# Kernel optimization log

Hardware: AMD Instinct MI355X
Metric: run time of the kernel (lower is better)

The kernel has to match this reference:

```python
import jax, jax.numpy as jnp
import numpy as np

N_NODES = 100000
N_EDGES = 1600000
IN_C, HID, OUT_C = 128, 64, 64
N_LAYERS = 16
ALPHA, THETA = 0.1, 0.5


def setup_inputs() -> dict:
    key = jax.random.key(0)
    ks = jax.random.split(key, 8)
    x = jax.random.normal(ks[0], (N_NODES, IN_C), dtype=jnp.float32)
    edge_index = jax.random.randint(ks[1], (2, N_EDGES), 0, N_NODES, dtype=jnp.int64)
    # torch Linear: weight [out, in], bias [out]
    lin0_w = jax.random.normal(ks[2], (HID, IN_C), dtype=jnp.float32) / np.sqrt(IN_C)
    lin0_b = jnp.zeros((HID,), dtype=jnp.float32)
    lin1_w = jax.random.normal(ks[3], (OUT_C, HID), dtype=jnp.float32) / np.sqrt(HID)
    lin1_b = jnp.zeros((OUT_C,), dtype=jnp.float32)
    # GCN2Conv weight1 per layer: [HID, HID], applied as h @ W
    conv_w = jax.random.normal(ks[4], (N_LAYERS, HID, HID), dtype=jnp.float32) / np.sqrt(HID)
    return {"x": x, "edge_index": edge_index, "lin0_w": lin0_w, "lin0_b": lin0_b,
            "lin1_w": lin1_w, "lin1_b": lin1_b, "conv_w": conv_w}


def reference(x, edge_index, lin0_w, lin0_b, lin1_w, lin1_b, conv_w):
    src, dst = edge_index[0], edge_index[1]
    # input projection (dropout p=0 in eval -> identity)
    h = jax.nn.relu(x @ lin0_w.T + lin0_b)  # [N, HID]
    h0 = h
    for l in range(N_LAYERS):
        # unweighted sum aggregation over edges (normalize=False, edge_weight=None)
        agg = jax.ops.segment_sum(h[src], dst, num_segments=N_NODES)  # [N, HID]
        z = (1.0 - ALPHA) * agg + ALPHA * h0  # initial residual
        beta = np.log(THETA / (l + 1) + 1.0).astype(np.float32)  # identity mapping strength
        h = jax.nn.relu((1.0 - beta) * z + beta * (z @ conv_w[l]))
    return h @ lin1_w.T + lin1_b  # [N, OUT_C]
```

## Files before the change

kernel.cpp:

```cpp
#include <hip/hip_runtime.h>
#include <cmath>

#define HID 64
#define IN_C 128

__device__ __forceinline__ float rl(float v, int k) {
    return __uint_as_float(__builtin_amdgcn_readlane(__float_as_uint(v), k));
}
__device__ __forceinline__ float bflo(unsigned u) { return __uint_as_float(u << 16); }
__device__ __forceinline__ float bfhi(unsigned u) { return __uint_as_float(u & 0xffff0000u); }
__device__ __forceinline__ unsigned bfpack(float lo, float hi) {
    unsigned a = __float_as_uint(lo), b = __float_as_uint(hi);
    a = (a + 0x7fffu + ((a >> 16) & 1u)) >> 16;
    b = (b + 0x7fffu + ((b >> 16) & 1u)) & 0xffff0000u;
    return a | b;
}

__device__ __forceinline__ float xadd8(float x) {
    int t = __builtin_amdgcn_update_dpp(0, __float_as_int(x), 0x128, 0xF, 0xF, true);
    return x + __int_as_float(t);
}
#if __has_builtin(__builtin_amdgcn_permlane16_swap)
typedef unsigned uvec2 __attribute__((ext_vector_type(2)));
__device__ __forceinline__ float xadd16(float x) {
    uvec2 r = __builtin_amdgcn_permlane16_swap(__float_as_uint(x), __float_as_uint(x), false, false);
    return __uint_as_float(r[0]) + __uint_as_float(r[1]);
}
#else
__device__ __forceinline__ float xadd16(float x) { return x + __shfl_xor(x, 16); }
#endif
#if __has_builtin(__builtin_amdgcn_permlane32_swap)
typedef unsigned uvec2b __attribute__((ext_vector_type(2)));
__device__ __forceinline__ float xadd32(float x) {
    uvec2b r = __builtin_amdgcn_permlane32_swap(__float_as_uint(x), __float_as_uint(x), false, false);
    return __uint_as_float(r[0]) + __uint_as_float(r[1]);
}
#else
__device__ __forceinline__ float xadd32(float x) { return x + __shfl_xor(x, 32); }
#endif
__device__ __forceinline__ float pairswap(float x) {
    int t = __builtin_amdgcn_update_dpp(0, __float_as_int(x), 0xB1, 0xF, 0xF, true);
    return __int_as_float(t);
}


__global__ void k_hist(const int* __restrict__ dst, int* __restrict__ counts, int E) {
    int e = blockIdx.x * blockDim.x + threadIdx.x;
    if (e < E) atomicAdd(&counts[dst[e]], 1);
}

__global__ void k_scan_block(const int* __restrict__ counts, int* __restrict__ row_ptr,
                             int* __restrict__ chunk_sums, int n) {
    __shared__ int s[1024];
    int i = blockIdx.x * 1024 + threadIdx.x;
    int v = (i < n) ? counts[i] : 0;
    s[threadIdx.x] = v;
    __syncthreads();
    for (int off = 1; off < 1024; off <<= 1) {
        int t = (threadIdx.x >= off) ? s[threadIdx.x - off] : 0;
        __syncthreads();
        s[threadIdx.x] += t;
        __syncthreads();
    }
    if (i < n) row_ptr[i] = s[threadIdx.x] - v;
    if (threadIdx.x == 1023) chunk_sums[blockIdx.x] = s[1023];
}

__global__ void k_scan_fix(int* __restrict__ row_ptr, const int* __restrict__ chunk_sums,
                           int n, int total) {
    __shared__ int base_s;
    if (threadIdx.x == 0) {
        int b = 0;
        for (int c = 0; c < (int)blockIdx.x; ++c) b += chunk_sums[c];
        base_s = b;
    }
    __syncthreads();
    int i = blockIdx.x * 1024 + threadIdx.x;
    if (i < n) row_ptr[i] += base_s;
    if (i == 0) row_ptr[n] = total;
}

__global__ void k_fill(const int* __restrict__ src, const int* __restrict__ dst,
                       const int* __restrict__ row_ptr, int* __restrict__ cursor,
                       int* __restrict__ col_idx, int E) {
    int e = blockIdx.x * blockDim.x + threadIdx.x;
    if (e < E) {
        int d = dst[e];
        int pos = row_ptr[d] + atomicAdd(&cursor[d], 1);
        col_idx[pos] = src[e];
    }
}

__global__ __launch_bounds__(256) void k_lin0(const float* __restrict__ x,
                                              const float* __restrict__ w,
                                              const float* __restrict__ b,
                                              unsigned* __restrict__ h0, int N) {
    __shared__ float Wt[IN_C * 65];
    for (int i = threadIdx.x; i < IN_C * HID; i += 256) {
        int o = i >> 7, k = i & 127;
        Wt[k * 65 + o] = w[i];
    }
    __syncthreads();
    int lane = threadIdx.x & 63;
    int wid = (blockIdx.x * blockDim.x + threadIdx.x) >> 6;
    int nw = (gridDim.x * blockDim.x) >> 6;
    float bias = b[lane];
    for (int n0 = wid; n0 < N; n0 += 2 * nw) {
        int n1 = n0 + nw;
        bool v1 = n1 < N;
        int n1c = v1 ? n1 : n0;
        float xa0 = x[(size_t)n0 * IN_C + lane];
        float xa1 = x[(size_t)n0 * IN_C + 64 + lane];
        float xb0 = x[(size_t)n1c * IN_C + lane];
        float xb1 = x[(size_t)n1c * IN_C + 64 + lane];
        float acc0 = bias, acc1 = bias;
#pragma unroll
        for (int k = 0; k < 64; ++k) {
            float wv = Wt[k * 65 + lane];
            acc0 = fmaf(rl(xa0, k), wv, acc0);
            acc1 = fmaf(rl(xb0, k), wv, acc1);
        }
#pragma unroll
        for (int k = 0; k < 64; ++k) {
            float wv = Wt[(64 + k) * 65 + lane];
            acc0 = fmaf(rl(xa1, k), wv, acc0);
            acc1 = fmaf(rl(xb1, k), wv, acc1);
        }
        acc0 = fmaxf(acc0, 0.f);
        acc1 = fmaxf(acc1, 0.f);
        float p0 = pairswap(acc0);
        float p1 = pairswap(acc1);
        if ((lane & 1) == 0) {
            h0[(size_t)n0 * 32 + (lane >> 1)] = bfpack(acc0, p0);
            if (v1) h0[(size_t)n1 * 32 + (lane >> 1)] = bfpack(acc1, p1);
        }
    }
}

__device__ __forceinline__ void mask4(uint4& q, bool v) {
    q.x = v ? q.x : 0u; q.y = v ? q.y : 0u; q.z = v ? q.z : 0u; q.w = v ? q.w : 0u;
}
__device__ __forceinline__ void acc8(float* a, const uint4& q) {
    a[0] += bflo(q.x); a[1] += bfhi(q.x);
    a[2] += bflo(q.y); a[3] += bfhi(q.y);
    a[4] += bflo(q.z); a[5] += bfhi(q.z);
    a[6] += bflo(q.w); a[7] += bfhi(q.w);
}

__global__ __launch_bounds__(256) void k_layer(const uint4* __restrict__ hin,
                                               const uint4* __restrict__ h0,
                                               unsigned* __restrict__ hout,
                                               const float* __restrict__ W,
                                               const int* __restrict__ row_ptr,
                                               const int* __restrict__ col_idx,
                                               float beta, int N, int E) {
    __shared__ uint4 Wp[8 * 64];
    for (int idx = threadIdx.x; idx < 8 * 64; idx += 256) {
        int k8 = idx >> 6, c = idx & 63;
        float wv[8];
#pragma unroll
        for (int m = 0; m < 8; ++m) {
            int k = 8 * k8 + m;
            float v = beta * W[k * 64 + c];
            if (k == c) v += 1.f - beta;
            wv[m] = v;
        }
        uint4 p;
        p.x = bfpack(wv[0], wv[1]); p.y = bfpack(wv[2], wv[3]);
        p.z = bfpack(wv[4], wv[5]); p.w = bfpack(wv[6], wv[7]);
        Wp[idx] = p;
    }
    __syncthreads();

    int lane = threadIdx.x & 63;
    int sub = lane >> 3;
    int cg = lane & 7;
    int wid = (blockIdx.x * blockDim.x + threadIdx.x) >> 6;
    int nw = (gridDim.x * blockDim.x) >> 6;

    for (int n = wid; n < N; n += 2 * nw) {
        int nB = n + nw;
        bool vB = nB < N;
        int nBc = vB ? nB : n;
        int bA = row_ptr[n];
        int dA = row_ptr[n + 1] - bA;
        int bB = row_ptr[nBc];
        int dB = vB ? row_ptr[nBc + 1] - bB : 0;
        uint4 hqA = h0[(size_t)n * 8 + cg];
        uint4 hqB = h0[(size_t)nBc * 8 + cg];
        int lastA = max(bA + dA - 1, 0);
        int lastB = max(bB + dB - 1, 0);
        float aA[8], aB[8];
#pragma unroll
        for (int c = 0; c < 8; ++c) { aA[c] = 0.f; aB[c] = 0.f; }
        int rmax = max(dA, dB);
        for (int j = 0; j < rmax; j += 16) {
            int p0 = j + sub, p1 = j + 8 + sub;
            int iA0 = col_idx[min(bA + p0, lastA)];
            int iA1 = col_idx[min(bA + p1, lastA)];
            int iB0 = col_idx[min(bB + p0, lastB)];
            int iB1 = col_idx[min(bB + p1, lastB)];
            uint4 qA0 = hin[(size_t)iA0 * 8 + cg];
            uint4 qA1 = hin[(size_t)iA1 * 8 + cg];
            uint4 qB0 = hin[(size_t)iB0 * 8 + cg];
            uint4 qB1 = hin[(size_t)iB1 * 8 + cg];
            mask4(qA0, p0 < dA); mask4(qA1, p1 < dA);
            mask4(qB0, p0 < dB); mask4(qB1, p1 < dB);
            acc8(aA, qA0); acc8(aA, qA1);
            acc8(aB, qB0); acc8(aB, qB1);
        }
#pragma unroll
        for (int c = 0; c < 8; ++c) { aA[c] = xadd8(aA[c]);  aB[c] = xadd8(aB[c]); }
#pragma unroll
        for (int c = 0; c < 8; ++c) { aA[c] = xadd16(aA[c]); aB[c] = xadd16(aB[c]); }
#pragma unroll
        for (int c = 0; c < 8; ++c) { aA[c] = xadd32(aA[c]); aB[c] = xadd32(aB[c]); }

        float zA[8], zB[8];
        zA[0] = 0.9f * aA[0] + 0.1f * bflo(hqA.x);
        zA[1] = 0.9f * aA[1] + 0.1f * bfhi(hqA.x);
        zA[2] = 0.9f * aA[2] + 0.1f * bflo(hqA.y);
        zA[3] = 0.9f * aA[3] + 0.1f * bfhi(hqA.y);
        zA[4] = 0.9f * aA[4] + 0.1f * bflo(hqA.z);
        zA[5] = 0.9f * aA[5] + 0.1f * bfhi(hqA.z);
        zA[6] = 0.9f * aA[6] + 0.1f * bflo(hqA.w);
        zA[7] = 0.9f * aA[7] + 0.1f * bfhi(hqA.w);
        zB[0] = 0.9f * aB[0] + 0.1f * bflo(hqB.x);
        zB[1] = 0.9f * aB[1] + 0.1f * bfhi(hqB.x);
        zB[2] = 0.9f * aB[2] + 0.1f * bflo(hqB.y);
        zB[3] = 0.9f * aB[3] + 0.1f * bfhi(hqB.y);
        zB[4] = 0.9f * aB[4] + 0.1f * bflo(hqB.z);
        zB[5] = 0.9f * aB[5] + 0.1f * bfhi(hqB.z);
        zB[6] = 0.9f * aB[6] + 0.1f * bflo(hqB.w);
        zB[7] = 0.9f * aB[7] + 0.1f * bfhi(hqB.w);

        float gA0 = 0.f, gA1 = 0.f, gA2 = 0.f, gA3 = 0.f;
        float gB0 = 0.f, gB1 = 0.f, gB2 = 0.f, gB3 = 0.f;
#pragma unroll
        for (int k8 = 0; k8 < 8; ++k8) {
            uint4 wp = Wp[k8 * 64 + lane];
            gA0 = fmaf(rl(zA[0], k8), bflo(wp.x), gA0);
            gA1 = fmaf(rl(zA[1], k8), bfhi(wp.x), gA1);
            gA2 = fmaf(rl(zA[2], k8), bflo(wp.y), gA2);
            gA3 = fmaf(rl(zA[3], k8), bfhi(wp.y), gA3);
            gA0 = fmaf(rl(zA[4], k8), bflo(wp.z), gA0);
            gA1 = fmaf(rl(zA[5], k8), bfhi(wp.z), gA1);
            gA2 = fmaf(rl(zA[6], k8), bflo(wp.w), gA2);
            gA3 = fmaf(rl(zA[7], k8), bfhi(wp.w), gA3);
            gB0 = fmaf(rl(zB[0], k8), bflo(wp.x), gB0);
            gB1 = fmaf(rl(zB[1], k8), bfhi(wp.x), gB1);
            gB2 = fmaf(rl(zB[2], k8), bflo(wp.y), gB2);
            gB3 = fmaf(rl(zB[3], k8), bfhi(wp.y), gB3);
            gB0 = fmaf(rl(zB[4], k8), bflo(wp.z), gB0);
            gB1 = fmaf(rl(zB[5], k8), bfhi(wp.z), gB1);
            gB2 = fmaf(rl(zB[6], k8), bflo(wp.w), gB2);
            gB3 = fmaf(rl(zB[7], k8), bfhi(wp.w), gB3);
        }
        float rA = fmaxf((gA0 + gA1) + (gA2 + gA3), 0.f);
        float rB = fmaxf((gB0 + gB1) + (gB2 + gB3), 0.f);
        float rAn = pairswap(rA);
        float rBn = pairswap(rB);
        if ((lane & 1) == 0) {
            hout[(size_t)n * 32 + (lane >> 1)] = bfpack(rA, rAn);
            if (vB) hout[(size_t)nB * 32 + (lane >> 1)] = bfpack(rB, rBn);
        }
    }
}

__global__ __launch_bounds__(256) void k_lin1(const unsigned* __restrict__ h,
                                              const float* __restrict__ w,
                                              const float* __restrict__ b,
                                              float* __restrict__ out, int N) {
    __shared__ float Wt[HID * 65];
    for (int i = threadIdx.x; i < HID * HID; i += 256) {
        int o = i >> 6, k = i & 63;
        Wt[k * 65 + o] = w[i];
    }
    __syncthreads();
    int lane = threadIdx.x & 63;
    int wid = (blockIdx.x * blockDim.x + threadIdx.x) >> 6;
    int nw = (gridDim.x * blockDim.x) >> 6;
    float bias = b[lane];
    for (int n0 = wid; n0 < N; n0 += 2 * nw) {
        int n1 = n0 + nw;
        bool v1 = n1 < N;
        int n1c = v1 ? n1 : n0;
        unsigned ua = h[(size_t)n0 * 32 + (lane >> 1)];
        unsigned ub = h[(size_t)n1c * 32 + (lane >> 1)];
        float ha = (lane & 1) ? bfhi(ua) : bflo(ua);
        float hb = (lane & 1) ? bfhi(ub) : bflo(ub);
        float acc0 = bias, acc1 = bias;
#pragma unroll
        for (int k = 0; k < 64; ++k) {
            float wv = Wt[k * 65 + lane];
            acc0 = fmaf(rl(ha, k), wv, acc0);
            acc1 = fmaf(rl(hb, k), wv, acc1);
        }
        out[(size_t)n0 * HID + lane] = acc0;
        if (v1) out[(size_t)n1 * HID + lane] = acc1;
    }
}

extern "C" void kernel_launch(void* const* d_in, const int* in_sizes, int n_in,
                              void* d_out, int out_size, void* d_ws, size_t ws_size,
                              hipStream_t stream) {
    const float* x      = (const float*)d_in[0];
    const int*   ei     = (const int*)d_in[1];
    const float* lin0_w = (const float*)d_in[2];
    const float* lin0_b = (const float*)d_in[3];
    const float* lin1_w = (const float*)d_in[4];
    const float* lin1_b = (const float*)d_in[5];
    const float* conv_w = (const float*)d_in[6];

    int N = in_sizes[0] / IN_C;
    int E = in_sizes[1] / 2;
    const int* src = ei;
    const int* dst = ei + E;

    unsigned* h0 = (unsigned*)d_ws;
    unsigned* hA = h0 + (size_t)N * 32;
    unsigned* hB = hA + (size_t)N * 32;
    int* row_ptr    = (int*)(hB + (size_t)N * 32);
    int* cursor     = row_ptr + (N + 1);
    int* col_idx    = cursor + N;
    int* chunk_sums = col_idx + E;

    int nch = (N + 1023) / 1024;

    hipMemsetAsync(cursor, 0, (size_t)N * sizeof(int), stream);
    k_hist<<<(E + 255) / 256, 256, 0, stream>>>(dst, cursor, E);
    k_scan_block<<<nch, 1024, 0, stream>>>(cursor, row_ptr, chunk_sums, N);
    k_scan_fix<<<nch, 1024, 0, stream>>>(row_ptr, chunk_sums, N, E);
    hipMemsetAsync(cursor, 0, (size_t)N * sizeof(int), stream);
    k_fill<<<(E + 255) / 256, 256, 0, stream>>>(src, dst, row_ptr, cursor, col_idx, E);

    k_lin0<<<1024, 256, 0, stream>>>(x, lin0_w, lin0_b, h0, N);

    const unsigned* cur = h0;
    for (int l = 0; l < 16; ++l) {
        float beta = (float)log(0.5 / (double)(l + 1) + 1.0);
        unsigned* nxt = (l & 1) ? hB : hA;
        k_layer<<<2048, 256, 0, stream>>>((const uint4*)cur, (const uint4*)h0, nxt,
                                          conv_w + (size_t)l * HID * HID,
                                          row_ptr, col_idx, beta, N, E);
        cur = nxt;
    }

    k_lin1<<<1024, 256, 0, stream>>>(cur, lin1_w, lin1_b, (float*)d_out, N);
}
```

Measured before the change: 1.507 ms.

## Process contiguous node chunks per wave and stage neighbor indices in LDS

Each wave now handles a contiguous chunk of 13 nodes instead of striding nodes across the grid. It loads the row pointers once per chunk into lanes and broadcasts them with readlane. It also prefetches the chunk's col_idx range (up to 512 entries) into shared memory with coalesced loads, falling back to global memory beyond that. This is meant to cut scattered row_ptr and col_idx loads, at the cost of extra LDS use (8KB per block), which may lower occupancy, and an unsynchronized per-wave LDS fill.

```diff
diff --git a/kernel.cpp b/kernel.cpp
--- a/kernel.cpp
+++ b/kernel.cpp
@@ -3,9 +3,14 @@
 
 #define HID 64
 #define IN_C 128
+#define CHUNK 13
+#define IDXCAP 512
 
 __device__ __forceinline__ float rl(float v, int k) {
     return __uint_as_float(__builtin_amdgcn_readlane(__float_as_uint(v), k));
+}
+__device__ __forceinline__ int rli(int v, int k) {
+    return __builtin_amdgcn_readlane(v, k);
 }
 __device__ __forceinline__ float bflo(unsigned u) { return __uint_as_float(u << 16); }
 __device__ __forceinline__ float bfhi(unsigned u) { return __uint_as_float(u & 0xffff0000u); }
@@ -153,8 +158,9 @@
                                                const float* __restrict__ W,
                                                const int* __restrict__ row_ptr,
                                                const int* __restrict__ col_idx,
-                                               float beta, int N, int E) {
+                                               float beta, int N) {
     __shared__ uint4 Wp[8 * 64];
+    __shared__ int idxb[4][IDXCAP];
     for (int idx = threadIdx.x; idx < 8 * 64; idx += 256) {
         int k8 = idx >> 6, c = idx & 63;
         float wv[8];
@@ -173,96 +179,109 @@
     __syncthreads();
 
     int lane = threadIdx.x & 63;
+    int wslot = threadIdx.x >> 6;
     int sub = lane >> 3;
     int cg = lane & 7;
-    int wid = (blockIdx.x * blockDim.x + threadIdx.x) >> 6;
-    int nw = (gridDim.x * blockDim.x) >> 6;
-
-    for (int n = wid; n < N; n += 2 * nw) {
-        int nB = n + nw;
-        bool vB = nB < N;
-        int nBc = vB ? nB : n;
-        int bA = row_ptr[n];
-        int dA = row_ptr[n + 1] - bA;
-        int bB = row_ptr[nBc];
-        int dB = vB ? row_ptr[nBc + 1] - bB : 0;
-        uint4 hqA = h0[(size_t)n * 8 + cg];
-        uint4 hqB = h0[(size_t)nBc * 8 + cg];
-        int lastA = max(bA + dA - 1, 0);
-        int lastB = max(bB + dB - 1, 0);
-        float aA[8], aB[8];
-#pragma unroll
-        for (int c = 0; c < 8; ++c) { aA[c] = 0.f; aB[c] = 0.f; }
-        int rmax = max(dA, dB);
-        for (int j = 0; j < rmax; j += 16) {
-            int p0 = j + sub, p1 = j + 8 + sub;
-            int iA0 = col_idx[min(bA + p0, lastA)];
-            int iA1 = col_idx[min(bA + p1, lastA)];
-            int iB0 = col_idx[min(bB + p0, lastB)];
-            int iB1 = col_idx[min(bB + p1, lastB)];
-            uint4 qA0 = hin[(size_t)iA0 * 8 + cg];
-            uint4 qA1 = hin[(size_t)iA1 * 8 + cg];
-            uint4 qB0 = hin[(size_t)iB0 * 8 + cg];
-            uint4 qB1 = hin[(size_t)iB1 * 8 + cg];
-            mask4(qA0, p0 < dA); mask4(qA1, p1 < dA);
-            mask4(qB0, p0 < dB); mask4(qB1, p1 < dB);
-            acc8(aA, qA0); acc8(aA, qA1);
-            acc8(aB, qB0); acc8(aB, qB1);
-        }
-#pragma unroll
-        for (int c = 0; c < 8; ++c) { aA[c] = xadd8(aA[c]);  aB[c] = xadd8(aB[c]); }
-#pragma unroll
-        for (int c = 0; c < 8; ++c) { aA[c] = xadd16(aA[c]); aB[c] = xadd16(aB[c]); }
-#pragma unroll
-        for (int c = 0; c < 8; ++c) { aA[c] = xadd32(aA[c]); aB[c] = xadd32(aB[c]); }
-
-        float zA[8], zB[8];
-        zA[0] = 0.9f * aA[0] + 0.1f * bflo(hqA.x);
-        zA[1] = 0.9f * aA[1] + 0.1f * bfhi(hqA.x);
-        zA[2] = 0.9f * aA[2] + 0.1f * bflo(hqA.y);
-        zA[3] = 0.9f * aA[3] + 0.1f * bfhi(hqA.y);
-        zA[4] = 0.9f * aA[4] + 0.1f * bflo(hqA.z);
-        zA[5] = 0.9f * aA[5] + 0.1f * bfhi(hqA.z);
-        zA[6] = 0.9f * aA[6] + 0.1f * bflo(hqA.w);
-        zA[7] = 0.9f * aA[7] + 0.1f * bfhi(hqA.w);
-        zB[0] = 0.9f * aB[0] + 0.1f * bflo(hqB.x);
-        zB[1] = 0.9f * aB[1] + 0.1f * bfhi(hqB.x);
-        zB[2] = 0.9f * aB[2] + 0.1f * bflo(hqB.y);
-        zB[3] = 0.9f * aB[3] + 0.1f * bfhi(hqB.y);
-        zB[4] = 0.9f * aB[4] + 0.1f * bflo(hqB.z);
-        zB[5] = 0.9f * aB[5] + 0.1f * bfhi(hqB.z);
-        zB[6] = 0.9f * aB[6] + 0.1f * bflo(hqB.w);
-        zB[7] = 0.9f * aB[7] + 0.1f * bfhi(hqB.w);
-
-        float gA0 = 0.f, gA1 = 0.f, gA2 = 0.f, gA3 = 0.f;
-        float gB0 = 0.f, gB1 = 0.f, gB2 = 0.f, gB3 = 0.f;
-#pragma unroll
-        for (int k8 = 0; k8 < 8; ++k8) {
-            uint4 wp = Wp[k8 * 64 + lane];
-            gA0 = fmaf(rl(zA[0], k8), bflo(wp.x), gA0);
-            gA1 = fmaf(rl(zA[1], k8), bfhi(wp.x), gA1);
-            gA2 = fmaf(rl(zA[2], k8), bflo(wp.y), gA2);
-            gA3 = fmaf(rl(zA[3], k8), bfhi(wp.y), gA3);
-            gA0 = fmaf(rl(zA[4], k8), bflo(wp.z), gA0);
-            gA1 = fmaf(rl(zA[5], k8), bfhi(wp.z), gA1);
-            gA2 = fmaf(rl(zA[6], k8), bflo(wp.w), gA2);
-            gA3 = fmaf(rl(zA[7], k8), bfhi(wp.w), gA3);
-            gB0 = fmaf(rl(zB[0], k8), bflo(wp.x), gB0);
-            gB1 = fmaf(rl(zB[1], k8), bfhi(wp.x), gB1);
-            gB2 = fmaf(rl(zB[2], k8), bflo(wp.y), gB2);
-            gB3 = fmaf(rl(zB[3], k8), bfhi(wp.y), gB3);
-            gB0 = fmaf(rl(zB[4], k8), bflo(wp.z), gB0);
-            gB1 = fmaf(rl(zB[5], k8), bfhi(wp.z), gB1);
-            gB2 = fmaf(rl(zB[6], k8), bflo(wp.w), gB2);
-            gB3 = fmaf(rl(zB[7], k8), bfhi(wp.w), gB3);
-        }
-        float rA = fmaxf((gA0 + gA1) + (gA2 + gA3), 0.f);
-        float rB = fmaxf((gB0 + gB1) + (gB2 + gB3), 0.f);
-        float rAn = pairswap(rA);
-        float rBn = pairswap(rB);
-        if ((lane & 1) == 0) {
-            hout[(size_t)n * 32 + (lane >> 1)] = bfpack(rA, rAn);
-            if (vB) hout[(size_t)nB * 32 + (lane >> 1)] = bfpack(rB, rBn);
+    int gw = (blockIdx.x * blockDim.x + threadIdx.x) >> 6;
+    int nwv = (gridDim.x * blockDim.x) >> 6;
+
+    for (int chunk = gw; chunk * CHUNK < N; chunk += nwv) {
+        int n0 = chunk * CHUNK;
+        int cnt = min(CHUNK, N - n0);
+        int rp = row_ptr[n0 + min(lane, cnt)];
+        int base = rli(rp, 0);
+        int tot = rli(rp, cnt) - base;
+        int ncap = min(tot, IDXCAP);
+        for (int t = lane; t < ncap; t += 64) idxb[wslot][t] = col_idx[base + t];
+
+        for (int i = 0; i < cnt; i += 2) {
+            bool vB = (i + 1) < cnt;
+            int iB = vB ? (i + 1) : i;
+            int rA0 = rli(rp, i), rA1 = rli(rp, i + 1);
+            int rB0 = rli(rp, iB), rB1 = rli(rp, iB + 1);
+            int bA = rA0 - base, dA = rA1 - rA0;
+            int bB = rB0 - base, dB = vB ? rB1 - rB0 : 0;
+            int nA = n0 + i, nB = n0 + iB;
+            uint4 hqA = h0[(size_t)nA * 8 + cg];
+            uint4 hqB = h0[(size_t)nB * 8 + cg];
+            int lastA = max(bA + dA - 1, 0);
+            int lastB = max(bB + dB - 1, 0);
+            float aA[8], aB[8];
+#pragma unroll
+            for (int c = 0; c < 8; ++c) { aA[c] = 0.f; aB[c] = 0.f; }
+            int rmax = max(dA, dB);
+            for (int j = 0; j < rmax; j += 16) {
+                int p0 = j + sub, p1 = j + 8 + sub;
+                int sA0 = min(bA + p0, lastA), sA1 = min(bA + p1, lastA);
+                int sB0 = min(bB + p0, lastB), sB1 = min(bB + p1, lastB);
+                int iA0 = (sA0 < IDXCAP) ? idxb[wslot][sA0] : col_idx[base + sA0];
+                int iA1 = (sA1 < IDXCAP) ? idxb[wslot][sA1] : col_idx[base + sA1];
+                int iB0 = (sB0 < IDXCAP) ? idxb[wslot][sB0] : col_idx[base + sB0];
+                int iB1 = (sB1 < IDXCAP) ? idxb[wslot][sB1] : col_idx[base + sB1];
+                uint4 qA0 = hin[(size_t)iA0 * 8 + cg];
+                uint4 qA1 = hin[(size_t)iA1 * 8 + cg];
+                uint4 qB0 = hin[(size_t)iB0 * 8 + cg];
+                uint4 qB1 = hin[(size_t)iB1 * 8 + cg];
+                mask4(qA0, p0 < dA); mask4(qA1, p1 < dA);
+                mask4(qB0, p0 < dB); mask4(qB1, p1 < dB);
+                acc8(aA, qA0); acc8(aA, qA1);
+                acc8(aB, qB0); acc8(aB, qB1);
+            }
+#pragma unroll
+            for (int c = 0; c < 8; ++c) { aA[c] = xadd8(aA[c]);  aB[c] = xadd8(aB[c]); }
+#pragma unroll
+            for (int c = 0; c < 8; ++c) { aA[c] = xadd16(aA[c]); aB[c] = xadd16(aB[c]); }
+#pragma unroll
+            for (int c = 0; c < 8; ++c) { aA[c] = xadd32(aA[c]); aB[c] = xadd32(aB[c]); }
+
+            float zA[8], zB[8];
+            zA[0] = 0.9f * aA[0] + 0.1f * bflo(hqA.x);
+            zA[1] = 0.9f * aA[1] + 0.1f * bfhi(hqA.x);
+            zA[2] = 0.9f * aA[2] + 0.1f * bflo(hqA.y);
+            zA[3] = 0.9f * aA[3] + 0.1f * bfhi(hqA.y);
+            zA[4] = 0.9f * aA[4] + 0.1f * bflo(hqA.z);
+            zA[5] = 0.9f * aA[5] + 0.1f * bfhi(hqA.z);
+            zA[6] = 0.9f * aA[6] + 0.1f * bflo(hqA.w);
+            zA[7] = 0.9f * aA[7] + 0.1f * bfhi(hqA.w);
+            zB[0] = 0.9f * aB[0] + 0.1f * bflo(hqB.x);
+            zB[1] = 0.9f * aB[1] + 0.1f * bfhi(hqB.x);
+            zB[2] = 0.9f * aB[2] + 0.1f * bflo(hqB.y);
+            zB[3] = 0.9f * aB[3] + 0.1f * bfhi(hqB.y);
+            zB[4] = 0.9f * aB[4] + 0.1f * bflo(hqB.z);
+            zB[5] = 0.9f * aB[5] + 0.1f * bfhi(hqB.z);
+            zB[6] = 0.9f * aB[6] + 0.1f * bflo(hqB.w);
+            zB[7] = 0.9f * aB[7] + 0.1f * bfhi(hqB.w);
+
+            float gA0 = 0.f, gA1 = 0.f, gA2 = 0.f, gA3 = 0.f;
+            float gB0 = 0.f, gB1 = 0.f, gB2 = 0.f, gB3 = 0.f;
+#pragma unroll
+            for (int k8 = 0; k8 < 8; ++k8) {
+                uint4 wp = Wp[k8 * 64 + lane];
+                gA0 = fmaf(rl(zA[0], k8), bflo(wp.x), gA0);
+                gA1 = fmaf(rl(zA[1], k8), bfhi(wp.x), gA1);
+                gA2 = fmaf(rl(zA[2], k8), bflo(wp.y), gA2);
+                gA3 = fmaf(rl(zA[3], k8), bfhi(wp.y), gA3);
+                gA0 = fmaf(rl(zA[4], k8), bflo(wp.z), gA0);
+                gA1 = fmaf(rl(zA[5], k8), bfhi(wp.z), gA1);
+                gA2 = fmaf(rl(zA[6], k8), bflo(wp.w), gA2);
+                gA3 = fmaf(rl(zA[7], k8), bfhi(wp.w), gA3);
+                gB0 = fmaf(rl(zB[0], k8), bflo(wp.x), gB0);
+                gB1 = fmaf(rl(zB[1], k8), bfhi(wp.x), gB1);
+                gB2 = fmaf(rl(zB[2], k8), bflo(wp.y), gB2);
+                gB3 = fmaf(rl(zB[3], k8), bfhi(wp.y), gB3);
+                gB0 = fmaf(rl(zB[4], k8), bflo(wp.z), gB0);
+                gB1 = fmaf(rl(zB[5], k8), bfhi(wp.z), gB1);
+                gB2 = fmaf(rl(zB[6], k8), bflo(wp.w), gB2);
+                gB3 = fmaf(rl(zB[7], k8), bfhi(wp.w), gB3);
+            }
+            float rA = fmaxf((gA0 + gA1) + (gA2 + gA3), 0.f);
+            float rB = fmaxf((gB0 + gB1) + (gB2 + gB3), 0.f);
+            float rAn = pairswap(rA);
+            float rBn = pairswap(rB);
+            if ((lane & 1) == 0) {
+                hout[(size_t)nA * 32 + (lane >> 1)] = bfpack(rA, rAn);
+                if (vB) hout[(size_t)nB * 32 + (lane >> 1)] = bfpack(rB, rBn);
+            }
         }
     }
 }
@@ -342,7 +361,7 @@
         unsigned* nxt = (l & 1) ? hB : hA;
         k_layer<<<2048, 256, 0, stream>>>((const uint4*)cur, (const uint4*)h0, nxt,
                                           conv_w + (size_t)l * HID * HID,
-                                          row_ptr, col_idx, beta, N, E);
+                                          row_ptr, col_idx, beta, N);
         cur = nxt;
     }
 
```

Result: slower. 1.583 ms (+5.1%).

## Split layer into channel-sliced aggregation and separate GEMM kernels

Applied to the files above, without the earlier changes.

Node features are stored channel-group-major: 8 slabs of 16-byte bf16 chunks, one slab per group of 8 channels. Each aggregation block handles a single slab, so its random gathers hit a 1.6 MB working set that can stay in cache. A separate GEMM kernel applies the mixing weight and converts back to the sliced layout. The cost is an intermediate z buffer (stored in the output buffer) that must be written and re-read, twice as many launches per layer, and one extra bf16 rounding of z.

```diff
diff --git a/kernel.cpp b/kernel.cpp
--- a/kernel.cpp
+++ b/kernel.cpp
@@ -16,28 +16,11 @@
     return a | b;
 }
 
-__device__ __forceinline__ float xadd8(float x) {
-    int t = __builtin_amdgcn_update_dpp(0, __float_as_int(x), 0x128, 0xF, 0xF, true);
+template <int CTRL>
+__device__ __forceinline__ float dppadd(float x) {
+    int t = __builtin_amdgcn_update_dpp(0, __float_as_int(x), CTRL, 0xF, 0xF, true);
     return x + __int_as_float(t);
 }
-#if __has_builtin(__builtin_amdgcn_permlane16_swap)
-typedef unsigned uvec2 __attribute__((ext_vector_type(2)));
-__device__ __forceinline__ float xadd16(float x) {
-    uvec2 r = __builtin_amdgcn_permlane16_swap(__float_as_uint(x), __float_as_uint(x), false, false);
-    return __uint_as_float(r[0]) + __uint_as_float(r[1]);
-}
-#else
-__device__ __forceinline__ float xadd16(float x) { return x + __shfl_xor(x, 16); }
-#endif
-#if __has_builtin(__builtin_amdgcn_permlane32_swap)
-typedef unsigned uvec2b __attribute__((ext_vector_type(2)));
-__device__ __forceinline__ float xadd32(float x) {
-    uvec2b r = __builtin_amdgcn_permlane32_swap(__float_as_uint(x), __float_as_uint(x), false, false);
-    return __uint_as_float(r[0]) + __uint_as_float(r[1]);
-}
-#else
-__device__ __forceinline__ float xadd32(float x) { return x + __shfl_xor(x, 32); }
-#endif
 __device__ __forceinline__ float pairswap(float x) {
     int t = __builtin_amdgcn_update_dpp(0, __float_as_int(x), 0xB1, 0xF, 0xF, true);
     return __int_as_float(t);
@@ -94,17 +77,19 @@
 __global__ __launch_bounds__(256) void k_lin0(const float* __restrict__ x,
                                               const float* __restrict__ w,
                                               const float* __restrict__ b,
-                                              unsigned* __restrict__ h0, int N) {
+                                              unsigned* __restrict__ S, int N) {
     __shared__ float Wt[IN_C * 65];
     for (int i = threadIdx.x; i < IN_C * HID; i += 256) {
         int o = i >> 7, k = i & 127;
         Wt[k * 65 + o] = w[i];
     }
     __syncthreads();
+    size_t N4 = (size_t)N * 4;
     int lane = threadIdx.x & 63;
     int wid = (blockIdx.x * blockDim.x + threadIdx.x) >> 6;
     int nw = (gridDim.x * blockDim.x) >> 6;
     float bias = b[lane];
+    size_t waddr = (size_t)(lane >> 3) * N4 + ((lane >> 1) & 3);
     for (int n0 = wid; n0 < N; n0 += 2 * nw) {
         int n1 = n0 + nw;
         bool v1 = n1 < N;
@@ -131,29 +116,111 @@
         float p0 = pairswap(acc0);
         float p1 = pairswap(acc1);
         if ((lane & 1) == 0) {
-            h0[(size_t)n0 * 32 + (lane >> 1)] = bfpack(acc0, p0);
-            if (v1) h0[(size_t)n1 * 32 + (lane >> 1)] = bfpack(acc1, p1);
-        }
-    }
-}
-
-__device__ __forceinline__ void mask4(uint4& q, bool v) {
-    q.x = v ? q.x : 0u; q.y = v ? q.y : 0u; q.z = v ? q.z : 0u; q.w = v ? q.w : 0u;
-}
-__device__ __forceinline__ void acc8(float* a, const uint4& q) {
-    a[0] += bflo(q.x); a[1] += bfhi(q.x);
-    a[2] += bflo(q.y); a[3] += bfhi(q.y);
-    a[4] += bflo(q.z); a[5] += bfhi(q.z);
-    a[6] += bflo(q.w); a[7] += bfhi(q.w);
-}
-
-__global__ __launch_bounds__(256) void k_layer(const uint4* __restrict__ hin,
-                                               const uint4* __restrict__ h0,
-                                               unsigned* __restrict__ hout,
-                                               const float* __restrict__ W,
-                                               const int* __restrict__ row_ptr,
-                                               const int* __restrict__ col_idx,
-                                               float beta, int N, int E) {
+            S[waddr + (size_t)n0 * 4] = bfpack(acc0, p0);
+            if (v1) S[waddr + (size_t)n1 * 4] = bfpack(acc1, p1);
+        }
+    }
+}
+
+__global__ __launch_bounds__(256) void k_aggr(const unsigned* __restrict__ Sin,
+                                              const unsigned* __restrict__ h0S,
+                                              unsigned* __restrict__ zrow,
+                                              const int* __restrict__ row_ptr,
+                                              const int* __restrict__ col_idx,
+                                              int N) {
+    int lane = threadIdx.x & 63;
+    int es = lane & 15, ds = lane >> 4;
+    int cg = blockIdx.x & 7;
+    int grp = blockIdx.x >> 3;
+    int ngrp = gridDim.x >> 3;
+    int wv = threadIdx.x >> 6;
+    int span = (N + ngrp - 1) / ngrp;
+    int nbeg = grp * span;
+    int nend = min(nbeg + span, N);
+    const uint4* slab = (const uint4*)(Sin + (size_t)cg * N * 4);
+    const uint4* h0sl = (const uint4*)(h0S + (size_t)cg * N * 4);
+    uint4* zr = (uint4*)zrow;
+
+    for (int n8 = nbeg + wv * 8; n8 < nend; n8 += 32) {
+        int nA = n8 + ds;
+        int nB = n8 + 4 + ds;
+        bool vA = nA < nend, vB = nB < nend;
+        int nAc = vA ? nA : nend - 1;
+        int nBc = vB ? nB : nend - 1;
+        int bA = row_ptr[nAc], eA = row_ptr[nAc + 1];
+        int bB = row_ptr[nBc], eB = row_ptr[nBc + 1];
+        int dA = eA - bA, dB = eB - bB;
+        int lastA = (dA > 0) ? eA - 1 : 0;
+        int lastB = (dB > 0) ? eB - 1 : 0;
+        int baseA = (dA > 0) ? bA : 0;
+        int baseB = (dB > 0) ? bB : 0;
+        float aA[8], aB[8];
+#pragma unroll
+        for (int c = 0; c < 8; ++c) { aA[c] = 0.f; aB[c] = 0.f; }
+        int rmax = max(dA, dB);
+        for (int j = es; j < rmax; j += 16) {
+            int pA = min(baseA + j, lastA);
+            int pB = min(baseB + j, lastB);
+            int iA = col_idx[pA];
+            int iB = col_idx[pB];
+            uint4 qA = slab[iA];
+            uint4 qB = slab[iB];
+            bool mA = j < dA, mB = j < dB;
+            if (!mA) { qA.x = 0; qA.y = 0; qA.z = 0; qA.w = 0; }
+            if (!mB) { qB.x = 0; qB.y = 0; qB.z = 0; qB.w = 0; }
+            aA[0] += bflo(qA.x); aA[1] += bfhi(qA.x);
+            aA[2] += bflo(qA.y); aA[3] += bfhi(qA.y);
+            aA[4] += bflo(qA.z); aA[5] += bfhi(qA.z);
+            aA[6] += bflo(qA.w); aA[7] += bfhi(qA.w);
+            aB[0] += bflo(qB.x); aB[1] += bfhi(qB.x);
+            aB[2] += bflo(qB.y); aB[3] += bfhi(qB.y);
+            aB[4] += bflo(qB.z); aB[5] += bfhi(qB.z);
+            aB[6] += bflo(qB.w); aB[7] += bfhi(qB.w);
+        }
+#pragma unroll
+        for (int c = 0; c < 8; ++c) { aA[c] = dppadd<0xB1>(aA[c]);  aB[c] = dppadd<0xB1>(aB[c]); }
+#pragma unroll
+        for (int c = 0; c < 8; ++c) { aA[c] = dppadd<0x4E>(aA[c]);  aB[c] = dppadd<0x4E>(aB[c]); }
+#pragma unroll
+        for (int c = 0; c < 8; ++c) { aA[c] = dppadd<0x124>(aA[c]); aB[c] = dppadd<0x124>(aB[c]); }
+#pragma unroll
+        for (int c = 0; c < 8; ++c) { aA[c] = dppadd<0x128>(aA[c]); aB[c] = dppadd<0x128>(aB[c]); }
+
+        uint4 hA = h0sl[nAc];
+        uint4 hB = h0sl[nBc];
+        float zA[8], zB[8];
+        zA[0] = 0.9f * aA[0] + 0.1f * bflo(hA.x);
+        zA[1] = 0.9f * aA[1] + 0.1f * bfhi(hA.x);
+        zA[2] = 0.9f * aA[2] + 0.1f * bflo(hA.y);
+        zA[3] = 0.9f * aA[3] + 0.1f * bfhi(hA.y);
+        zA[4] = 0.9f * aA[4] + 0.1f * bflo(hA.z);
+        zA[5] = 0.9f * aA[5] + 0.1f * bfhi(hA.z);
+        zA[6] = 0.9f * aA[6] + 0.1f * bflo(hA.w);
+        zA[7] = 0.9f * aA[7] + 0.1f * bfhi(hA.w);
+        zB[0] = 0.9f * aB[0] + 0.1f * bflo(hB.x);
+        zB[1] = 0.9f * aB[1] + 0.1f * bfhi(hB.x);
+        zB[2] = 0.9f * aB[2] + 0.1f * bflo(hB.y);
+        zB[3] = 0.9f * aB[3] + 0.1f * bfhi(hB.y);
+        zB[4] = 0.9f * aB[4] + 0.1f * bflo(hB.z);
+        zB[5] = 0.9f * aB[5] + 0.1f * bfhi(hB.z);
+        zB[6] = 0.9f * aB[6] + 0.1f * bflo(hB.w);
+        zB[7] = 0.9f * aB[7] + 0.1f * bfhi(hB.w);
+        uint4 zqA, zqB;
+        zqA.x = bfpack(zA[0], zA[1]); zqA.y = bfpack(zA[2], zA[3]);
+        zqA.z = bfpack(zA[4], zA[5]); zqA.w = bfpack(zA[6], zA[7]);
+        zqB.x = bfpack(zB[0], zB[1]); zqB.y = bfpack(zB[2], zB[3]);
+        zqB.z = bfpack(zB[4], zB[5]); zqB.w = bfpack(zB[6], zB[7]);
+        if (es == 0) {
+            if (vA) zr[(size_t)nA * 8 + cg] = zqA;
+            if (vB) zr[(size_t)nB * 8 + cg] = zqB;
+        }
+    }
+}
+
+__global__ __launch_bounds__(256) void k_gemm(const uint4* __restrict__ zrow,
+                                              unsigned* __restrict__ Sout,
+                                              const float* __restrict__ W,
+                                              float beta, int N) {
     __shared__ uint4 Wp[8 * 64];
     for (int idx = threadIdx.x; idx < 8 * 64; idx += 256) {
         int k8 = idx >> 6, c = idx & 63;
@@ -172,67 +239,28 @@
     }
     __syncthreads();
 
+    size_t N4 = (size_t)N * 4;
     int lane = threadIdx.x & 63;
-    int sub = lane >> 3;
     int cg = lane & 7;
     int wid = (blockIdx.x * blockDim.x + threadIdx.x) >> 6;
     int nw = (gridDim.x * blockDim.x) >> 6;
-
-    for (int n = wid; n < N; n += 2 * nw) {
-        int nB = n + nw;
-        bool vB = nB < N;
-        int nBc = vB ? nB : n;
-        int bA = row_ptr[n];
-        int dA = row_ptr[n + 1] - bA;
-        int bB = row_ptr[nBc];
-        int dB = vB ? row_ptr[nBc + 1] - bB : 0;
-        uint4 hqA = h0[(size_t)n * 8 + cg];
-        uint4 hqB = h0[(size_t)nBc * 8 + cg];
-        int lastA = max(bA + dA - 1, 0);
-        int lastB = max(bB + dB - 1, 0);
-        float aA[8], aB[8];
-#pragma unroll
-        for (int c = 0; c < 8; ++c) { aA[c] = 0.f; aB[c] = 0.f; }
-        int rmax = max(dA, dB);
-        for (int j = 0; j < rmax; j += 16) {
-            int p0 = j + sub, p1 = j + 8 + sub;
-            int iA0 = col_idx[min(bA + p0, lastA)];
-            int iA1 = col_idx[min(bA + p1, lastA)];
-            int iB0 = col_idx[min(bB + p0, lastB)];
-            int iB1 = col_idx[min(bB + p1, lastB)];
-            uint4 qA0 = hin[(size_t)iA0 * 8 + cg];
-            uint4 qA1 = hin[(size_t)iA1 * 8 + cg];
-            uint4 qB0 = hin[(size_t)iB0 * 8 + cg];
-            uint4 qB1 = hin[(size_t)iB1 * 8 + cg];
-            mask4(qA0, p0 < dA); mask4(qA1, p1 < dA);
-            mask4(qB0, p0 < dB); mask4(qB1, p1 < dB);
-            acc8(aA, qA0); acc8(aA, qA1);
-            acc8(aB, qB0); acc8(aB, qB1);
-        }
-#pragma unroll
-        for (int c = 0; c < 8; ++c) { aA[c] = xadd8(aA[c]);  aB[c] = xadd8(aB[c]); }
-#pragma unroll
-        for (int c = 0; c < 8; ++c) { aA[c] = xadd16(aA[c]); aB[c] = xadd16(aB[c]); }
-#pragma unroll
-        for (int c = 0; c < 8; ++c) { aA[c] = xadd32(aA[c]); aB[c] = xadd32(aB[c]); }
-
+    size_t waddr = (size_t)(lane >> 3) * N4 + ((lane >> 1) & 3);
+
+    for (int n0 = 2 * wid; n0 < N; n0 += 2 * nw) {
+        int n1 = n0 + 1;
+        bool v1 = n1 < N;
+        int n1c = v1 ? n1 : n0;
+        uint4 zqA = zrow[(size_t)n0 * 8 + cg];
+        uint4 zqB = zrow[(size_t)n1c * 8 + cg];
         float zA[8], zB[8];
-        zA[0] = 0.9f * aA[0] + 0.1f * bflo(hqA.x);
-        zA[1] = 0.9f * aA[1] + 0.1f * bfhi(hqA.x);
-        zA[2] = 0.9f * aA[2] + 0.1f * bflo(hqA.y);
-        zA[3] = 0.9f * aA[3] + 0.1f * bfhi(hqA.y);
-        zA[4] = 0.9f * aA[4] + 0.1f * bflo(hqA.z);
-        zA[5] = 0.9f * aA[5] + 0.1f * bfhi(hqA.z);
-        zA[6] = 0.9f * aA[6] + 0.1f * bflo(hqA.w);
-        zA[7] = 0.9f * aA[7] + 0.1f * bfhi(hqA.w);
-        zB[0] = 0.9f * aB[0] + 0.1f * bflo(hqB.x);
-        zB[1] = 0.9f * aB[1] + 0.1f * bfhi(hqB.x);
-        zB[2] = 0.9f * aB[2] + 0.1f * bflo(hqB.y);
-        zB[3] = 0.9f * aB[3] + 0.1f * bfhi(hqB.y);
-        zB[4] = 0.9f * aB[4] + 0.1f * bflo(hqB.z);
-        zB[5] = 0.9f * aB[5] + 0.1f * bfhi(hqB.z);
-        zB[6] = 0.9f * aB[6] + 0.1f * bflo(hqB.w);
-        zB[7] = 0.9f * aB[7] + 0.1f * bfhi(hqB.w);
+        zA[0] = bflo(zqA.x); zA[1] = bfhi(zqA.x);
+        zA[2] = bflo(zqA.y); zA[3] = bfhi(zqA.y);
+        zA[4] = bflo(zqA.z); zA[5] = bfhi(zqA.z);
+        zA[6] = bflo(zqA.w); zA[7] = bfhi(zqA.w);
+        zB[0] = bflo(zqB.x); zB[1] = bfhi(zqB.x);
+        zB[2] = bflo(zqB.y); zB[3] = bfhi(zqB.y);
+        zB[4] = bflo(zqB.z); zB[5] = bfhi(zqB.z);
+        zB[6] = bflo(zqB.w); zB[7] = bfhi(zqB.w);
 
         float gA0 = 0.f, gA1 = 0.f, gA2 = 0.f, gA3 = 0.f;
         float gB0 = 0.f, gB1 = 0.f, gB2 = 0.f, gB3 = 0.f;
@@ -261,13 +289,13 @@
         float rAn = pairswap(rA);
         float rBn = pairswap(rB);
         if ((lane & 1) == 0) {
-            hout[(size_t)n * 32 + (lane >> 1)] = bfpack(rA, rAn);
-            if (vB) hout[(size_t)nB * 32 + (lane >> 1)] = bfpack(rB, rBn);
-        }
-    }
-}
-
-__global__ __launch_bounds__(256) void k_lin1(const unsigned* __restrict__ h,
+            Sout[waddr + (size_t)n0 * 4] = bfpack(rA, rAn);
+            if (v1) Sout[waddr + (size_t)n1 * 4] = bfpack(rB, rBn);
+        }
+    }
+}
+
+__global__ __launch_bounds__(256) void k_lin1(const unsigned* __restrict__ S,
                                               const float* __restrict__ w,
                                               const float* __restrict__ b,
                                               float* __restrict__ out, int N) {
@@ -277,16 +305,18 @@
         Wt[k * 65 + o] = w[i];
     }
     __syncthreads();
+    size_t N4 = (size_t)N * 4;
     int lane = threadIdx.x & 63;
     int wid = (blockIdx.x * blockDim.x + threadIdx.x) >> 6;
     int nw = (gridDim.x * blockDim.x) >> 6;
     float bias = b[lane];
+    size_t raddr = (size_t)(lane >> 3) * N4 + ((lane >> 1) & 3);
     for (int n0 = wid; n0 < N; n0 += 2 * nw) {
         int n1 = n0 + nw;
         bool v1 = n1 < N;
         int n1c = v1 ? n1 : n0;
-        unsigned ua = h[(size_t)n0 * 32 + (lane >> 1)];
-        unsigned ub = h[(size_t)n1c * 32 + (lane >> 1)];
+        unsigned ua = S[raddr + (size_t)n0 * 4];
+        unsigned ub = S[raddr + (size_t)n1c * 4];
         float ha = (lane & 1) ? bfhi(ua) : bflo(ua);
         float hb = (lane & 1) ? bfhi(ub) : bflo(ub);
         float acc0 = bias, acc1 = bias;
@@ -317,13 +347,14 @@
     const int* src = ei;
     const int* dst = ei + E;
 
-    unsigned* h0 = (unsigned*)d_ws;
-    unsigned* hA = h0 + (size_t)N * 32;
-    unsigned* hB = hA + (size_t)N * 32;
-    int* row_ptr    = (int*)(hB + (size_t)N * 32);
+    unsigned* h0S = (unsigned*)d_ws;
+    unsigned* SA  = h0S + (size_t)N * 32;
+    unsigned* SB  = SA + (size_t)N * 32;
+    int* row_ptr    = (int*)(SB + (size_t)N * 32);
     int* cursor     = row_ptr + (N + 1);
     int* col_idx    = cursor + N;
     int* chunk_sums = col_idx + E;
+    unsigned* Z = (unsigned*)d_out;
 
     int nch = (N + 1023) / 1024;
 
@@ -334,15 +365,15 @@
     hipMemsetAsync(cursor, 0, (size_t)N * sizeof(int), stream);
     k_fill<<<(E + 255) / 256, 256, 0, stream>>>(src, dst, row_ptr, cursor, col_idx, E);
 
-    k_lin0<<<1024, 256, 0, stream>>>(x, lin0_w, lin0_b, h0, N);
-
-    const unsigned* cur = h0;
+    k_lin0<<<1024, 256, 0, stream>>>(x, lin0_w, lin0_b, h0S, N);
+
+    const unsigned* cur = h0S;
     for (int l = 0; l < 16; ++l) {
         float beta = (float)log(0.5 / (double)(l + 1) + 1.0);
-        unsigned* nxt = (l & 1) ? hB : hA;
-        k_layer<<<2048, 256, 0, stream>>>((const uint4*)cur, (const uint4*)h0, nxt,
-                                          conv_w + (size_t)l * HID * HID,
-                                          row_ptr, col_idx, beta, N, E);
+        unsigned* nxt = (l & 1) ? SB : SA;
+        k_aggr<<<1024, 256, 0, stream>>>(cur, h0S, Z, row_ptr, col_idx, N);
+        k_gemm<<<2048, 256, 0, stream>>>((const uint4*)Z, nxt,
+                                         conv_w + (size_t)l * HID * HID, beta, N);
         cur = nxt;
     }
 
```

New measurement: 2.254 ms. 49.6% more time.
